# Kernel tuning notes

Hardware: AMD Instinct MI355X
Metric: run time of the kernel (lower is better)

Reference implementation:

```python
import jax, jax.numpy as jnp
import numpy as np

N, E, IN, HID, H, L, CLS = 10000, 160000, 512, 128, 8, 4, 2
ALPHA = 0.1  # residual weight
BN_EPS = 1e-5
NEG_SLOPE = 0.2  # PyG GATConv leaky_relu default


def setup_inputs() -> dict:
    key = jax.random.key(0)
    ks = jax.random.split(key, 16)
    s = 0.05
    return {
        "x": jax.random.normal(ks[0], (N, IN), jnp.float32),
        "edge_index": jax.random.randint(ks[1], (2, E), 0, N, jnp.int64),
        "Wp": jax.random.normal(ks[2], (IN, HID), jnp.float32) * s,
        "bp": jax.random.normal(ks[3], (HID,), jnp.float32) * s,
        # stacked per-layer GATConv params (shared src/dst weight as in PyG)
        "Wl": jax.random.normal(ks[4], (L, HID, H * HID), jnp.float32) * s,
        "att_src": jax.random.normal(ks[5], (L, H, HID), jnp.float32) * s,
        "att_dst": jax.random.normal(ks[6], (L, H, HID), jnp.float32) * s,
        "bl": jax.random.normal(ks[7], (L, HID), jnp.float32) * s,
        # BatchNorm (eval mode: running_mean=0, running_var=1)
        "gamma": 1.0 + jax.random.normal(ks[8], (L, HID), jnp.float32) * s,
        "beta": jax.random.normal(ks[9], (L, HID), jnp.float32) * s,
        # classifier
        "W1": jax.random.normal(ks[10], (HID, HID // 2), jnp.float32) * s,
        "b1": jax.random.normal(ks[11], (HID // 2,), jnp.float32) * s,
        "W2": jax.random.normal(ks[12], (HID // 2, CLS), jnp.float32) * s,
        "b2": jax.random.normal(ks[13], (CLS,), jnp.float32) * s,
    }


def gat_layer(h, src, dst, W, a_src, a_dst, bias):
    # h: [N, HID]; W: [HID, H*HID]
    xl = (h @ W).reshape(N, H, HID)                 # [N, H, C]
    alpha_s = jnp.sum(xl * a_src[None], axis=-1)     # [N, H]
    alpha_d = jnp.sum(xl * a_dst[None], axis=-1)     # [N, H]
    e = jax.nn.leaky_relu(alpha_s[src] + alpha_d[dst], NEG_SLOPE)  # [E', H]
    # segment softmax over incoming edges of each dst node
    emax = jax.ops.segment_max(e, dst, num_segments=N)
    ee = jnp.exp(e - emax[dst])
    denom = jax.ops.segment_sum(ee, dst, num_segments=N)
    att = ee / (denom[dst] + 1e-16)                  # [E', H]
    msg = xl[src] * att[:, :, None]                  # [E', H, C]
    out = jax.ops.segment_sum(msg, dst, num_segments=N)  # [N, H, C]
    return out.mean(axis=1) + bias                   # concat=False -> mean over heads


def reference(x, edge_index, Wp, bp, Wl, att_src, att_dst, bl, gamma, beta, W1, b1, W2, b2):
    # add self-loops (PyG GATConv default add_self_loops=True)
    loop = jnp.arange(N, dtype=edge_index.dtype)
    src = jnp.concatenate([edge_index[0], loop])
    dst = jnp.concatenate([edge_index[1], loop])

    h = jax.nn.elu(x @ Wp + bp)
    bn_inv = 1.0 / jnp.sqrt(1.0 + BN_EPS)
    for i in range(L):
        prev = h
        g = gat_layer(h, src, dst, Wl[i], att_src[i], att_dst[i], bl[i])
        g = gamma[i] * (g * bn_inv) + beta[i]        # BN eval (mean 0, var 1)
        h = jax.nn.elu((1.0 - ALPHA) * g + ALPHA * prev)
        # dropout is identity in eval mode
    hid = jax.nn.elu(h @ W1 + b1)
    return hid @ W2 + b2                             # [N, CLS]
```

## Files before the change

### kernel.cpp

```cpp
#include <hip/hip_runtime.h>
#include <cstdint>
#include <cstddef>

#define N_NODES 10000
#define N_EDGES 160000
#define DIM_IN  512
#define HIDDIM  128
#define NHEAD   8
#define NLAYER  4

typedef unsigned int   uint32;
typedef unsigned short ushort16;
typedef __attribute__((ext_vector_type(8))) short bf16x8;
typedef __attribute__((ext_vector_type(4))) float f32x4;

static __device__ __forceinline__ float eluf(float v)  { return v > 0.f ? v : expm1f(v); }
static __device__ __forceinline__ float lrelu(float v) { return v >= 0.f ? v : 0.2f * v; }
static __device__ __forceinline__ ushort16 f2bf(float f) {
    uint32 u = __float_as_uint(f);
    u += 0x7fffu + ((u >> 16) & 1u);
    return (ushort16)(u >> 16);
}
static __device__ __forceinline__ float blo(uint32 u) { return __uint_as_float(u << 16); }
static __device__ __forceinline__ float bhi(uint32 u) { return __uint_as_float(u & 0xffff0000u); }

#define BN_INV 0.9999950000374997f

__global__ void k_deg(const int* __restrict__ ei, int* __restrict__ deg) {
    int t = blockIdx.x * 256 + threadIdx.x;
    if (t < N_EDGES) atomicAdd(&deg[ei[N_EDGES + t]], 1);
}

__global__ __launch_bounds__(1024) void k_scan(const int* __restrict__ deg,
                                               int* __restrict__ rowptr,
                                               int* __restrict__ cursor) {
    __shared__ int sd[1024];
    __shared__ int carry;
    int tid = threadIdx.x;
    if (tid == 0) { carry = 0; rowptr[0] = 0; }
    __syncthreads();
    for (int base = 0; base < N_NODES; base += 1024) {
        int i = base + tid;
        int v = (i < N_NODES) ? (deg[i] + 1) : 0;
        sd[tid] = v;
        __syncthreads();
        for (int ofs = 1; ofs < 1024; ofs <<= 1) {
            int t = (tid >= ofs) ? sd[tid - ofs] : 0;
            __syncthreads();
            sd[tid] += t;
            __syncthreads();
        }
        int inc = sd[tid] + carry;
        if (i < N_NODES) { rowptr[i + 1] = inc; cursor[i] = inc - v; }
        __syncthreads();
        if (tid == 1023) carry = inc;
        __syncthreads();
    }
}

__global__ void k_scatter(const int* __restrict__ ei, int* __restrict__ cursor,
                          int* __restrict__ csr) {
    int t = blockIdx.x * 256 + threadIdx.x;
    if (t < N_EDGES) {
        int s = ei[t];
        int d = ei[N_EDGES + t];
        int p = atomicAdd(&cursor[d], 1);
        csr[p] = s;
    } else if (t < N_EDGES + N_NODES) {
        int n = t - N_EDGES;
        int p = atomicAdd(&cursor[n], 1);
        csr[p] = n;
    }
}

template <int ACT, int OUTBF>
__global__ __launch_bounds__(256) void k_gemm_mfma(const float* __restrict__ A,
                                                   const float* __restrict__ B,
                                                   const float* __restrict__ bias,
                                                   void* __restrict__ Cv,
                                                   int M, int Nn, int K) {
    __shared__ unsigned short AsU[64 * 128];
    __shared__ unsigned short BsU[64 * 128];
    char* AsB = (char*)AsU;
    char* BsB = (char*)BsU;
    const int tid = threadIdx.x;
    const int lane = tid & 63;
    const int wv = tid >> 6;
    const int row0 = blockIdx.y * 64, col0 = blockIdx.x * 64;
    const int r = lane & 15, q = lane >> 4;

    f32x4 acc[4];
#pragma unroll
    for (int i = 0; i < 4; i++) acc[i] = (f32x4){0.f, 0.f, 0.f, 0.f};

    for (int k0 = 0; k0 < K; k0 += 128) {
        __syncthreads();
#pragma unroll
        for (int it = 0; it < 8; it++) {
            int gq = tid + it * 256;
            int row = gq >> 5;
            int k4 = (gq & 31) * 4;
            int gr = row0 + row;
            float4 v = make_float4(0.f, 0.f, 0.f, 0.f);
            if (gr < M) v = *(const float4*)(A + (size_t)gr * K + k0 + k4);
            ushort4 o;
            o.x = f2bf(v.x); o.y = f2bf(v.y); o.z = f2bf(v.z); o.w = f2bf(v.w);
            int byte = (row * 256 + k4 * 2) ^ ((row & 7) << 4);
            *(ushort4*)(AsB + byte) = o;
        }
#pragma unroll
        for (int it = 0; it < 8; it++) {
            int gq = tid + it * 256;
            int kk = gq >> 4;
            int c4 = (gq & 15) * 4;
            float4 v = *(const float4*)(B + (size_t)(k0 + kk) * Nn + col0 + c4);
            float vv[4] = {v.x, v.y, v.z, v.w};
#pragma unroll
            for (int c = 0; c < 4; c++) {
                int col = c4 + c;
                int byte = (col * 256 + kk * 2) ^ ((col & 7) << 4);
                *(unsigned short*)(BsB + byte) = f2bf(vv[c]);
            }
        }
        __syncthreads();
#pragma unroll
        for (int ks = 0; ks < 4; ks++) {
            int kb = (ks * 32 + q * 8) * 2;
            int arow = wv * 16 + r;
            bf16x8 af = *(bf16x8*)(AsB + ((arow * 256 + kb) ^ ((arow & 7) << 4)));
#pragma unroll
            for (int nb = 0; nb < 4; nb++) {
                int col = nb * 16 + r;
                bf16x8 bfr = *(bf16x8*)(BsB + ((col * 256 + kb) ^ ((col & 7) << 4)));
                acc[nb] = __builtin_amdgcn_mfma_f32_16x16x32_bf16(af, bfr, acc[nb], 0, 0, 0);
            }
        }
    }
#pragma unroll
    for (int nb = 0; nb < 4; nb++) {
        int col = col0 + nb * 16 + r;
#pragma unroll
        for (int j = 0; j < 4; j++) {
            int row = row0 + wv * 16 + q * 4 + j;
            if (row < M) {
                float v = acc[nb][j];
                if (ACT) { v += bias[col]; v = eluf(v); }
                if (OUTBF) ((unsigned short*)Cv)[(size_t)row * Nn + col] = f2bf(v);
                else       ((float*)Cv)[(size_t)row * Nn + col] = v;
            }
        }
    }
}

__global__ __launch_bounds__(256) void k_alphas(const ushort16* __restrict__ xl,
                                                const float* __restrict__ atts,
                                                const float* __restrict__ attd,
                                                float* __restrict__ as_,
                                                float* __restrict__ ad_) {
    int lane = threadIdx.x & 63;
    int n = blockIdx.x * 4 + (threadIdx.x >> 6);
    if (n >= N_NODES) return;
    int g = lane >> 4;
    int c8 = 8 * (lane & 15);
    const uint4* xp = (const uint4*)(xl + (size_t)n * 1024);
    float ss[2], sd[2];
#pragma unroll
    for (int j = 0; j < 2; j++) {
        int head = 4 * j + g;
        uint4 u = xp[j * 64 + lane];
        const float4* ap = (const float4*)(atts + head * 128 + c8);
        const float4* bp = (const float4*)(attd + head * 128 + c8);
        float4 a0 = ap[0], a1 = ap[1];
        float4 b0 = bp[0], b1 = bp[1];
        float x0 = blo(u.x), x1 = bhi(u.x), x2 = blo(u.y), x3 = bhi(u.y);
        float x4 = blo(u.z), x5 = bhi(u.z), x6 = blo(u.w), x7 = bhi(u.w);
        ss[j] = x0 * a0.x + x1 * a0.y + x2 * a0.z + x3 * a0.w +
                x4 * a1.x + x5 * a1.y + x6 * a1.z + x7 * a1.w;
        sd[j] = x0 * b0.x + x1 * b0.y + x2 * b0.z + x3 * b0.w +
                x4 * b1.x + x5 * b1.y + x6 * b1.z + x7 * b1.w;
    }
#pragma unroll
    for (int m = 1; m < 16; m <<= 1) {
#pragma unroll
        for (int j = 0; j < 2; j++) {
            ss[j] += __shfl_xor(ss[j], m);
            sd[j] += __shfl_xor(sd[j], m);
        }
    }
    if ((lane & 15) == 0) {
        as_[n * 8 + g]     = ss[0];
        as_[n * 8 + 4 + g] = ss[1];
        ad_[n * 8 + g]     = sd[0];
        ad_[n * 8 + 4 + g] = sd[1];
    }
}

__global__ __launch_bounds__(256) void k_aggregate(const int* __restrict__ rowptr,
                                                   const int* __restrict__ csr,
                                                   const float* __restrict__ as_,
                                                   const float* __restrict__ ad_,
                                                   const ushort16* __restrict__ xl,
                                                   const float* __restrict__ hprev,
                                                   const float* __restrict__ bl,
                                                   const float* __restrict__ gam,
                                                   const float* __restrict__ bet,
                                                   float* __restrict__ hnext) {
    int lane = threadIdx.x & 63;
    int n = blockIdx.x * 4 + (threadIdx.x >> 6);
    if (n >= N_NODES) return;
    int h8 = lane & 7;
    int g = lane >> 4;
    float adh = ad_[n * 8 + h8];
    int start = rowptr[n], end = rowptr[n + 1];

    float acc0[8] = {}, acc1[8] = {};
    float denom = 0.f;
    int e = start;
    int s0 = csr[e];
    int s1 = (e + 1 < end) ? csr[e + 1] : 0;
    for (; e + 1 < end; e += 2) {
        int s2 = (e + 2 < end) ? csr[e + 2] : 0;
        int s3 = (e + 3 < end) ? csr[e + 3] : 0;
        float as0 = as_[s0 * 8 + h8];
        float as1 = as_[s1 * 8 + h8];
        const uint4* xp0 = (const uint4*)(xl + (size_t)s0 * 1024);
        const uint4* xp1 = (const uint4*)(xl + (size_t)s1 * 1024);
        uint4 u0a = xp0[lane], u1a = xp0[64 + lane];
        uint4 u0b = xp1[lane], u1b = xp1[64 + lane];
        float ee0 = __expf(lrelu(as0 + adh));
        float ee1 = __expf(lrelu(as1 + adh));
        denom += ee0 + ee1;
        float e0a = __shfl(ee0, g), e1a = __shfl(ee0, 4 + g);
        float e0b = __shfl(ee1, g), e1b = __shfl(ee1, 4 + g);
        acc0[0] += e0a * blo(u0a.x); acc0[1] += e0a * bhi(u0a.x);
        acc0[2] += e0a * blo(u0a.y); acc0[3] += e0a * bhi(u0a.y);
        acc0[4] += e0a * blo(u0a.z); acc0[5] += e0a * bhi(u0a.z);
        acc0[6] += e0a * blo(u0a.w); acc0[7] += e0a * bhi(u0a.w);
        acc1[0] += e1a * blo(u1a.x); acc1[1] += e1a * bhi(u1a.x);
        acc1[2] += e1a * blo(u1a.y); acc1[3] += e1a * bhi(u1a.y);
        acc1[4] += e1a * blo(u1a.z); acc1[5] += e1a * bhi(u1a.z);
        acc1[6] += e1a * blo(u1a.w); acc1[7] += e1a * bhi(u1a.w);
        acc0[0] += e0b * blo(u0b.x); acc0[1] += e0b * bhi(u0b.x);
        acc0[2] += e0b * blo(u0b.y); acc0[3] += e0b * bhi(u0b.y);
        acc0[4] += e0b * blo(u0b.z); acc0[5] += e0b * bhi(u0b.z);
        acc0[6] += e0b * blo(u0b.w); acc0[7] += e0b * bhi(u0b.w);
        acc1[0] += e1b * blo(u1b.x); acc1[1] += e1b * bhi(u1b.x);
        acc1[2] += e1b * blo(u1b.y); acc1[3] += e1b * bhi(u1b.y);
        acc1[4] += e1b * blo(u1b.z); acc1[5] += e1b * bhi(u1b.z);
        acc1[6] += e1b * blo(u1b.w); acc1[7] += e1b * bhi(u1b.w);
        s0 = s2; s1 = s3;
    }
    if (e < end) {
        float as0 = as_[s0 * 8 + h8];
        const uint4* xp0 = (const uint4*)(xl + (size_t)s0 * 1024);
        uint4 u0a = xp0[lane], u1a = xp0[64 + lane];
        float ee0 = __expf(lrelu(as0 + adh));
        denom += ee0;
        float e0a = __shfl(ee0, g), e1a = __shfl(ee0, 4 + g);
        acc0[0] += e0a * blo(u0a.x); acc0[1] += e0a * bhi(u0a.x);
        acc0[2] += e0a * blo(u0a.y); acc0[3] += e0a * bhi(u0a.y);
        acc0[4] += e0a * blo(u0a.z); acc0[5] += e0a * bhi(u0a.z);
        acc0[6] += e0a * blo(u0a.w); acc0[7] += e0a * bhi(u0a.w);
        acc1[0] += e1a * blo(u1a.x); acc1[1] += e1a * bhi(u1a.x);
        acc1[2] += e1a * blo(u1a.y); acc1[3] += e1a * bhi(u1a.y);
        acc1[4] += e1a * blo(u1a.z); acc1[5] += e1a * bhi(u1a.z);
        acc1[6] += e1a * blo(u1a.w); acc1[7] += e1a * bhi(u1a.w);
    }

    float d0 = __shfl(denom, g);
    float d1 = __shfl(denom, 4 + g);
    float r0 = 1.f / (d0 + 1e-16f);
    float r1 = 1.f / (d1 + 1e-16f);
    float sum[8];
#pragma unroll
    for (int i = 0; i < 8; i++) sum[i] = acc0[i] * r0 + acc1[i] * r1;
#pragma unroll
    for (int i = 0; i < 8; i++) {
        sum[i] += __shfl_xor(sum[i], 16);
        sum[i] += __shfl_xor(sum[i], 32);
    }

    if (lane < 16) {
        int c = 8 * lane;
        float o[8];
#pragma unroll
        for (int t = 0; t < 8; t++) {
            float m = sum[t] * 0.125f + bl[c + t];
            float gg = gam[c + t] * (m * BN_INV) + bet[c + t];
            float z = 0.9f * gg + 0.1f * hprev[(size_t)n * 128 + c + t];
            o[t] = eluf(z);
        }
        *(float4*)(hnext + (size_t)n * 128 + c)     = make_float4(o[0], o[1], o[2], o[3]);
        *(float4*)(hnext + (size_t)n * 128 + c + 4) = make_float4(o[4], o[5], o[6], o[7]);
    }
}

__global__ __launch_bounds__(256) void k_classifier(const float* __restrict__ h,
                                                    const float* __restrict__ W1,
                                                    const float* __restrict__ b1,
                                                    const float* __restrict__ W2,
                                                    const float* __restrict__ b2,
                                                    float* __restrict__ out) {
    __shared__ float sW1[128 * 64];
    __shared__ float sW2[128];
    __shared__ float sb1[64];
    __shared__ float sb2[2];
    for (int i = threadIdx.x; i < 2048; i += 256)
        *(float4*)&sW1[i * 4] = *(const float4*)(W1 + i * 4);
    if (threadIdx.x < 64) sb1[threadIdx.x] = b1[threadIdx.x];
    if (threadIdx.x < 128) sW2[threadIdx.x] = W2[threadIdx.x];
    if (threadIdx.x < 2) sb2[threadIdx.x] = b2[threadIdx.x];
    __syncthreads();
    int lane = threadIdx.x & 63;
    int n = blockIdx.x * 4 + (threadIdx.x >> 6);
    if (n >= N_NODES) return;
    float h0 = h[(size_t)n * 128 + lane];
    float h1 = h[(size_t)n * 128 + 64 + lane];
    float acc = sb1[lane];
#pragma unroll
    for (int c = 0; c < 64; c++) acc += __shfl(h0, c) * sW1[c * 64 + lane];
#pragma unroll
    for (int c = 0; c < 64; c++) acc += __shfl(h1, c) * sW1[(64 + c) * 64 + lane];
    acc = eluf(acc);
    float p0 = acc * sW2[lane * 2 + 0];
    float p1 = acc * sW2[lane * 2 + 1];
#pragma unroll
    for (int m = 1; m < 64; m <<= 1) {
        p0 += __shfl_xor(p0, m);
        p1 += __shfl_xor(p1, m);
    }
    if (lane == 0) {
        out[(size_t)n * 2 + 0] = p0 + sb2[0];
        out[(size_t)n * 2 + 1] = p1 + sb2[1];
    }
}

extern "C" void kernel_launch(void* const* d_in, const int* in_sizes, int n_in,
                              void* d_out, int out_size, void* d_ws, size_t ws_size,
                              hipStream_t stream) {
    const float* x       = (const float*)d_in[0];
    const int* ei        = (const int*)d_in[1];
    const float* Wp      = (const float*)d_in[2];
    const float* bp      = (const float*)d_in[3];
    const float* Wl      = (const float*)d_in[4];
    const float* atts    = (const float*)d_in[5];
    const float* attd    = (const float*)d_in[6];
    const float* bl      = (const float*)d_in[7];
    const float* gam     = (const float*)d_in[8];
    const float* bet     = (const float*)d_in[9];
    const float* W1      = (const float*)d_in[10];
    const float* b1      = (const float*)d_in[11];
    const float* W2      = (const float*)d_in[12];
    const float* b2      = (const float*)d_in[13];
    float* out = (float*)d_out;

    char* w = (char*)d_ws;
    auto carve = [&](size_t bytes) -> void* {
        void* p = (void*)w;
        w += (bytes + 255) & ~(size_t)255;
        return p;
    };
    int* deg        = (int*)carve((size_t)N_NODES * 4);
    int* rowptr     = (int*)carve((size_t)(N_NODES + 1) * 4);
    int* cursor     = (int*)carve((size_t)N_NODES * 4);
    int* csr        = (int*)carve((size_t)(N_EDGES + N_NODES) * 4);
    float* as_      = (float*)carve((size_t)N_NODES * 8 * 4);
    float* ad_      = (float*)carve((size_t)N_NODES * 8 * 4);
    ushort16* xl    = (ushort16*)carve((size_t)N_NODES * 1024 * 2);
    float* hA       = (float*)carve((size_t)N_NODES * 128 * 4);
    float* hB       = (float*)carve((size_t)N_NODES * 128 * 4);

    hipMemsetAsync(deg, 0, (size_t)N_NODES * 4, stream);
    k_deg<<<(N_EDGES + 255) / 256, 256, 0, stream>>>(ei, deg);
    k_scan<<<1, 1024, 0, stream>>>(deg, rowptr, cursor);
    k_scatter<<<(N_EDGES + N_NODES + 255) / 256, 256, 0, stream>>>(ei, cursor, csr);

    k_gemm_mfma<1, 0><<<dim3(2, 157), 256, 0, stream>>>(x, Wp, bp, hA, N_NODES, 128, 512);

    float* hc = hA;
    float* hn = hB;
    for (int l = 0; l < NLAYER; l++) {
        k_gemm_mfma<0, 1><<<dim3(16, 157), 256, 0, stream>>>(hc, Wl + (size_t)l * 128 * 1024,
                                                             nullptr, xl, N_NODES, 1024, 128);
        k_alphas<<<2500, 256, 0, stream>>>(xl, atts + l * 1024, attd + l * 1024, as_, ad_);
        k_aggregate<<<2500, 256, 0, stream>>>(rowptr, csr, as_, ad_, xl, hc, bl + l * 128,
                                              gam + l * 128, bet + l * 128, hn);
        float* tmp = hc; hc = hn; hn = tmp;
    }
    k_classifier<<<2500, 256, 0, stream>>>(hc, W1, b1, W2, b2, out);
}
```

Before: 504.3 us.

## Fuse attention logit computation into GEMM epilogue and unroll aggregation by four

Computes per-head source and destination attention logits directly from the GEMM accumulators using shuffle reductions and atomics, removing the separate alphas kernel and its re-read of the projected features. A memset per layer zeroes the logit buffers before accumulation. The aggregation loop now processes four edges per iteration to expose more outstanding gathers. Atomics add some contention and the logits now come from unrounded fp32 values rather than bf16, slightly changing numerics.

```diff
diff --git a/kernel.cpp b/kernel.cpp
--- a/kernel.cpp
+++ b/kernel.cpp
@@ -73,11 +73,15 @@
     }
 }
 
-template <int ACT, int OUTBF>
+template <int ACT, int OUTBF, int ALPHA>
 __global__ __launch_bounds__(256) void k_gemm_mfma(const float* __restrict__ A,
                                                    const float* __restrict__ B,
                                                    const float* __restrict__ bias,
                                                    void* __restrict__ Cv,
+                                                   const float* __restrict__ atts,
+                                                   const float* __restrict__ attd,
+                                                   float* __restrict__ as_,
+                                                   float* __restrict__ ad_,
                                                    int M, int Nn, int K) {
     __shared__ unsigned short AsU[64 * 128];
     __shared__ unsigned short BsU[64 * 128];
@@ -150,48 +154,36 @@
             }
         }
     }
-}
-
-__global__ __launch_bounds__(256) void k_alphas(const ushort16* __restrict__ xl,
-                                                const float* __restrict__ atts,
-                                                const float* __restrict__ attd,
-                                                float* __restrict__ as_,
-                                                float* __restrict__ ad_) {
-    int lane = threadIdx.x & 63;
-    int n = blockIdx.x * 4 + (threadIdx.x >> 6);
-    if (n >= N_NODES) return;
-    int g = lane >> 4;
-    int c8 = 8 * (lane & 15);
-    const uint4* xp = (const uint4*)(xl + (size_t)n * 1024);
-    float ss[2], sd[2];
-#pragma unroll
-    for (int j = 0; j < 2; j++) {
-        int head = 4 * j + g;
-        uint4 u = xp[j * 64 + lane];
-        const float4* ap = (const float4*)(atts + head * 128 + c8);
-        const float4* bp = (const float4*)(attd + head * 128 + c8);
-        float4 a0 = ap[0], a1 = ap[1];
-        float4 b0 = bp[0], b1 = bp[1];
-        float x0 = blo(u.x), x1 = bhi(u.x), x2 = blo(u.y), x3 = bhi(u.y);
-        float x4 = blo(u.z), x5 = bhi(u.z), x6 = blo(u.w), x7 = bhi(u.w);
-        ss[j] = x0 * a0.x + x1 * a0.y + x2 * a0.z + x3 * a0.w +
-                x4 * a1.x + x5 * a1.y + x6 * a1.z + x7 * a1.w;
-        sd[j] = x0 * b0.x + x1 * b0.y + x2 * b0.z + x3 * b0.w +
-                x4 * b1.x + x5 * b1.y + x6 * b1.z + x7 * b1.w;
-    }
-#pragma unroll
-    for (int m = 1; m < 16; m <<= 1) {
-#pragma unroll
-        for (int j = 0; j < 2; j++) {
-            ss[j] += __shfl_xor(ss[j], m);
-            sd[j] += __shfl_xor(sd[j], m);
-        }
-    }
-    if ((lane & 15) == 0) {
-        as_[n * 8 + g]     = ss[0];
-        as_[n * 8 + 4 + g] = ss[1];
-        ad_[n * 8 + g]     = sd[0];
-        ad_[n * 8 + 4 + g] = sd[1];
+    if (ALPHA) {
+        int hd = col0 >> 7;
+        int cb = col0 & 127;
+        float ws[4], wd[4];
+#pragma unroll
+        for (int nb = 0; nb < 4; nb++) {
+            ws[nb] = atts[hd * 128 + cb + nb * 16 + r];
+            wd[nb] = attd[hd * 128 + cb + nb * 16 + r];
+        }
+#pragma unroll
+        for (int j = 0; j < 4; j++) {
+            float ps = 0.f, pd = 0.f;
+#pragma unroll
+            for (int nb = 0; nb < 4; nb++) {
+                ps += acc[nb][j] * ws[nb];
+                pd += acc[nb][j] * wd[nb];
+            }
+#pragma unroll
+            for (int m = 1; m < 16; m <<= 1) {
+                ps += __shfl_xor(ps, m);
+                pd += __shfl_xor(pd, m);
+            }
+            if (r == 0) {
+                int row = row0 + wv * 16 + q * 4 + j;
+                if (row < M) {
+                    atomicAdd(&as_[row * 8 + hd], ps);
+                    atomicAdd(&ad_[row * 8 + hd], pd);
+                }
+            }
+        }
     }
 }
 
@@ -216,45 +208,50 @@
     float acc0[8] = {}, acc1[8] = {};
     float denom = 0.f;
     int e = start;
-    int s0 = csr[e];
-    int s1 = (e + 1 < end) ? csr[e + 1] : 0;
-    for (; e + 1 < end; e += 2) {
-        int s2 = (e + 2 < end) ? csr[e + 2] : 0;
-        int s3 = (e + 3 < end) ? csr[e + 3] : 0;
-        float as0 = as_[s0 * 8 + h8];
-        float as1 = as_[s1 * 8 + h8];
+    for (; e + 3 < end; e += 4) {
+        int s0 = csr[e], s1 = csr[e + 1], s2 = csr[e + 2], s3 = csr[e + 3];
+        float a0 = as_[s0 * 8 + h8], a1 = as_[s1 * 8 + h8];
+        float a2 = as_[s2 * 8 + h8], a3 = as_[s3 * 8 + h8];
         const uint4* xp0 = (const uint4*)(xl + (size_t)s0 * 1024);
         const uint4* xp1 = (const uint4*)(xl + (size_t)s1 * 1024);
+        const uint4* xp2 = (const uint4*)(xl + (size_t)s2 * 1024);
+        const uint4* xp3 = (const uint4*)(xl + (size_t)s3 * 1024);
         uint4 u0a = xp0[lane], u1a = xp0[64 + lane];
         uint4 u0b = xp1[lane], u1b = xp1[64 + lane];
-        float ee0 = __expf(lrelu(as0 + adh));
-        float ee1 = __expf(lrelu(as1 + adh));
-        denom += ee0 + ee1;
+        uint4 u0c = xp2[lane], u1c = xp2[64 + lane];
+        uint4 u0d = xp3[lane], u1d = xp3[64 + lane];
+        float ee0 = __expf(lrelu(a0 + adh));
+        float ee1 = __expf(lrelu(a1 + adh));
+        float ee2 = __expf(lrelu(a2 + adh));
+        float ee3 = __expf(lrelu(a3 + adh));
+        denom += (ee0 + ee1) + (ee2 + ee3);
         float e0a = __shfl(ee0, g), e1a = __shfl(ee0, 4 + g);
         float e0b = __shfl(ee1, g), e1b = __shfl(ee1, 4 + g);
-        acc0[0] += e0a * blo(u0a.x); acc0[1] += e0a * bhi(u0a.x);
-        acc0[2] += e0a * blo(u0a.y); acc0[3] += e0a * bhi(u0a.y);
-        acc0[4] += e0a * blo(u0a.z); acc0[5] += e0a * bhi(u0a.z);
-        acc0[6] += e0a * blo(u0a.w); acc0[7] += e0a * bhi(u0a.w);
-        acc1[0] += e1a * blo(u1a.x); acc1[1] += e1a * bhi(u1a.x);
-        acc1[2] += e1a * blo(u1a.y); acc1[3] += e1a * bhi(u1a.y);
-        acc1[4] += e1a * blo(u1a.z); acc1[5] += e1a * bhi(u1a.z);
-        acc1[6] += e1a * blo(u1a.w); acc1[7] += e1a * bhi(u1a.w);
-        acc0[0] += e0b * blo(u0b.x); acc0[1] += e0b * bhi(u0b.x);
-        acc0[2] += e0b * blo(u0b.y); acc0[3] += e0b * bhi(u0b.y);
-        acc0[4] += e0b * blo(u0b.z); acc0[5] += e0b * bhi(u0b.z);
-        acc0[6] += e0b * blo(u0b.w); acc0[7] += e0b * bhi(u0b.w);
-        acc1[0] += e1b * blo(u1b.x); acc1[1] += e1b * bhi(u1b.x);
-        acc1[2] += e1b * blo(u1b.y); acc1[3] += e1b * bhi(u1b.y);
-        acc1[4] += e1b * blo(u1b.z); acc1[5] += e1b * bhi(u1b.z);
-        acc1[6] += e1b * blo(u1b.w); acc1[7] += e1b * bhi(u1b.w);
-        s0 = s2; s1 = s3;
-    }
-    if (e < end) {
-        float as0 = as_[s0 * 8 + h8];
+        float e0c = __shfl(ee2, g), e1c = __shfl(ee2, 4 + g);
+        float e0d = __shfl(ee3, g), e1d = __shfl(ee3, 4 + g);
+        acc0[0] += e0a * blo(u0a.x) + e0b * blo(u0b.x) + e0c * blo(u0c.x) + e0d * blo(u0d.x);
+        acc0[1] += e0a * bhi(u0a.x) + e0b * bhi(u0b.x) + e0c * bhi(u0c.x) + e0d * bhi(u0d.x);
+        acc0[2] += e0a * blo(u0a.y) + e0b * blo(u0b.y) + e0c * blo(u0c.y) + e0d * blo(u0d.y);
+        acc0[3] += e0a * bhi(u0a.y) + e0b * bhi(u0b.y) + e0c * bhi(u0c.y) + e0d * bhi(u0d.y);
+        acc0[4] += e0a * blo(u0a.z) + e0b * blo(u0b.z) + e0c * blo(u0c.z) + e0d * blo(u0d.z);
+        acc0[5] += e0a * bhi(u0a.z) + e0b * bhi(u0b.z) + e0c * bhi(u0c.z) + e0d * bhi(u0d.z);
+        acc0[6] += e0a * blo(u0a.w) + e0b * blo(u0b.w) + e0c * blo(u0c.w) + e0d * blo(u0d.w);
+        acc0[7] += e0a * bhi(u0a.w) + e0b * bhi(u0b.w) + e0c * bhi(u0c.w) + e0d * bhi(u0d.w);
+        acc1[0] += e1a * blo(u1a.x) + e1b * blo(u1b.x) + e1c * blo(u1c.x) + e1d * blo(u1d.x);
+        acc1[1] += e1a * bhi(u1a.x) + e1b * bhi(u1b.x) + e1c * bhi(u1c.x) + e1d * bhi(u1d.x);
+        acc1[2] += e1a * blo(u1a.y) + e1b * blo(u1b.y) + e1c * blo(u1c.y) + e1d * blo(u1d.y);
+        acc1[3] += e1a * bhi(u1a.y) + e1b * bhi(u1b.y) + e1c * bhi(u1c.y) + e1d * bhi(u1d.y);
+        acc1[4] += e1a * blo(u1a.z) + e1b * blo(u1b.z) + e1c * blo(u1c.z) + e1d * blo(u1d.z);
+        acc1[5] += e1a * bhi(u1a.z) + e1b * bhi(u1b.z) + e1c * bhi(u1c.z) + e1d * bhi(u1d.z);
+        acc1[6] += e1a * blo(u1a.w) + e1b * blo(u1b.w) + e1c * blo(u1c.w) + e1d * blo(u1d.w);
+        acc1[7] += e1a * bhi(u1a.w) + e1b * bhi(u1b.w) + e1c * bhi(u1c.w) + e1d * bhi(u1d.w);
+    }
+    for (; e < end; ++e) {
+        int s0 = csr[e];
+        float a0 = as_[s0 * 8 + h8];
         const uint4* xp0 = (const uint4*)(xl + (size_t)s0 * 1024);
         uint4 u0a = xp0[lane], u1a = xp0[64 + lane];
-        float ee0 = __expf(lrelu(as0 + adh));
+        float ee0 = __expf(lrelu(a0 + adh));
         denom += ee0;
         float e0a = __shfl(ee0, g), e1a = __shfl(ee0, 4 + g);
         acc0[0] += e0a * blo(u0a.x); acc0[1] += e0a * bhi(u0a.x);
@@ -375,14 +372,16 @@
     k_scan<<<1, 1024, 0, stream>>>(deg, rowptr, cursor);
     k_scatter<<<(N_EDGES + N_NODES + 255) / 256, 256, 0, stream>>>(ei, cursor, csr);
 
-    k_gemm_mfma<1, 0><<<dim3(2, 157), 256, 0, stream>>>(x, Wp, bp, hA, N_NODES, 128, 512);
+    k_gemm_mfma<1, 0, 0><<<dim3(2, 157), 256, 0, stream>>>(
+        x, Wp, bp, hA, nullptr, nullptr, nullptr, nullptr, N_NODES, 128, 512);
 
     float* hc = hA;
     float* hn = hB;
     for (int l = 0; l < NLAYER; l++) {
-        k_gemm_mfma<0, 1><<<dim3(16, 157), 256, 0, stream>>>(hc, Wl + (size_t)l * 128 * 1024,
-                                                             nullptr, xl, N_NODES, 1024, 128);
-        k_alphas<<<2500, 256, 0, stream>>>(xl, atts + l * 1024, attd + l * 1024, as_, ad_);
+        hipMemsetAsync(as_, 0, (size_t)N_NODES * 8 * 4 * 2, stream);
+        k_gemm_mfma<0, 1, 1><<<dim3(16, 157), 256, 0, stream>>>(
+            hc, Wl + (size_t)l * 128 * 1024, nullptr, xl,
+            atts + l * 1024, attd + l * 1024, as_, ad_, N_NODES, 1024, 128);
         k_aggregate<<<2500, 256, 0, stream>>>(rowptr, csr, as_, ad_, xl, hc, bl + l * 128,
                                               gam + l * 128, bet + l * 128, hn);
         float* tmp = hc; hc = hn; hn = tmp;
```

Measured after the change: 544.1 us. +7.9%, slower.
